# Kernel optimization log

Measured on AMD Instinct MI355X. Metric: run time of the kernel, lower is better.

Reference implementation:

```python
import jax, jax.numpy as jnp
import numpy as np

N = 4096
IN_C, HID_C, OUT_C = 128, 256, 128


def setup_inputs() -> dict:
    key = jax.random.key(0)
    ks = jax.random.split(key, 6)
    return {
        "x": jax.random.normal(ks[0], (N, IN_C), jnp.float32),
        "attn_tensor": jax.random.normal(ks[1], (1, 12, N, N), jnp.float32),
        "agg_w": jax.random.normal(ks[2], (12,), jnp.float32),
        "agg_b": jax.random.normal(ks[3], (1,), jnp.float32),
        "W1": jax.random.normal(ks[4], (IN_C, HID_C), jnp.float32) * (IN_C ** -0.5),
        "b1": jnp.zeros((HID_C,), jnp.float32),
        "W2": jax.random.normal(ks[5], (HID_C, OUT_C), jnp.float32) * (HID_C ** -0.5),
        "b2": jnp.zeros((OUT_C,), jnp.float32),
    }


def reference(x, attn_tensor, agg_w, agg_b, W1, b1, W2, b2):
    # 1x1 conv over 12 channels -> [B, N, N]
    agg = jnp.einsum("bcuv,c->buv", attn_tensor, agg_w) + agg_b[0]
    # per-batch 0.9 quantile (torch.quantile default linear interpolation)
    thresh = jnp.quantile(agg.reshape(agg.shape[0], -1), 0.9, axis=1)
    mask = agg[0] >= thresh[0]                      # [N, N] boolean adjacency
    n = mask.shape[0]
    # dense adjacency; add remaining self-loops (PyG gcn_norm fill_value=1)
    A = jnp.maximum(mask.astype(x.dtype), jnp.eye(n, dtype=x.dtype))
    deg = A.sum(axis=0)                             # in-degree at target (col) index
    s = jnp.where(deg > 0, jax.lax.rsqrt(deg), 0.0)  # D^{-1/2}, inf -> 0

    def gcn(h, W, b):
        h = h @ W                                    # linear transform (no bias)
        # out[v] = s[v] * sum_u A[u, v] * s[u] * h[u]  (source->target flow)
        return s[:, None] * (A.T @ (s[:, None] * h)) + b

    h = jax.nn.relu(gcn(x, W1, b1))
    return gcn(h, W2, b2)
```

## Files before the change

kernel.cpp:

```cpp
#include <hip/hip_runtime.h>
#include <stdint.h>

#define N_NODES 4096
#define NNN ((int64_t)N_NODES * (int64_t)N_NODES)
#define TOTAL4 (NNN / 4)
#define NC 12
#define K0_RANK 15099493u

#define SROWS 164
#define SSTRIDE 25
#define LO_RANK 601210u
#define HI_RANK 607929u

#define M_SHIST 0
#define M_CH1   4096
#define M_CH2   4352
#define M_HB    8448
#define M_DEG   8704
#define M_CNTS  12800
#define M_BLO   13824
#define M_BHI   13825
#define M_NBEL  13826
#define M_MXM   13827
#define M_SELX  13828
#define M_WORDS 14336

#define CHUNK_V 16384

typedef __attribute__((ext_vector_type(2))) _Float16 half2v;
typedef __attribute__((ext_vector_type(4))) float f4v;

static __device__ __forceinline__ uint32_t f2key(float f) {
    uint32_t x = __float_as_uint(f);
    return (x & 0x80000000u) ? ~x : (x | 0x80000000u);
}
static __device__ __forceinline__ float key2f(uint32_t k) {
    uint32_t x = (k & 0x80000000u) ? (k & 0x7FFFFFFFu) : ~k;
    return __uint_as_float(x);
}

static __device__ __forceinline__ void select_bin(const uint32_t* __restrict__ gh,
        int nb, uint32_t target, uint32_t* hl, uint32_t* sc, uint32_t* out) {
    int t = threadIdx.x;
    int per = nb >> 8;
    for (int i = t; i < nb; i += 256) hl[i] = gh[i];
    __syncthreads();
    uint32_t p = 0;
    for (int i = 0; i < per; ++i) p += hl[t * per + i];
    sc[t] = p;
    __syncthreads();
    for (int d = 1; d < 256; d <<= 1) {
        uint32_t v = (t >= d) ? sc[t - d] : 0u;
        __syncthreads();
        sc[t] += v;
        __syncthreads();
    }
    uint32_t excl = sc[t] - p;
    if (p > 0 && target >= excl && target < excl + p) {
        uint32_t cum = excl; int b = t * per;
        while (cum + hl[b] <= target) { cum += hl[b]; ++b; }
        out[0] = (uint32_t)b; out[1] = target - cum;
    }
    __syncthreads();
}

__global__ __launch_bounds__(256) void sample_kernel(const float* __restrict__ attn,
        const float* __restrict__ w, const float* __restrict__ bb,
        uint32_t* __restrict__ meta, const float* __restrict__ x,
        _Float16* __restrict__ x_h) {
    {
        const float2* x2 = (const float2*)x;
        half2v* xh2 = (half2v*)x_h;
        for (int i = blockIdx.x * 256 + threadIdx.x; i < 262144; i += 256 * 256) {
            float2 v = x2[i];
            half2v h; h[0] = (_Float16)v.x; h[1] = (_Float16)v.y;
            xh2[i] = h;
        }
    }
    __shared__ uint32_t h[4096];
    for (int i = threadIdx.x; i < 4096; i += 256) h[i] = 0;
    float wr[NC];
#pragma unroll
    for (int c = 0; c < NC; ++c) wr[c] = w[c];
    float b0 = bb[0];
    __syncthreads();
    const f4v* a4 = (const f4v*)attn;
    for (int idx = blockIdx.x * 256 + threadIdx.x; idx < SROWS * 1024; idx += 256 * 256) {
        int r = idx >> 10;
        int64_t off = (int64_t)(r * SSTRIDE) * 1024 + (idx & 1023);
        float ax = b0, ay = b0, az = b0, aw = b0;
#pragma unroll
        for (int c = 0; c < NC; ++c) {
            f4v t = __builtin_nontemporal_load(a4 + (int64_t)c * TOTAL4 + off);
            ax += wr[c] * t.x; ay += wr[c] * t.y; az += wr[c] * t.z; aw += wr[c] * t.w;
        }
        atomicAdd(&h[f2key(ax) >> 20], 1u);
        atomicAdd(&h[f2key(ay) >> 20], 1u);
        atomicAdd(&h[f2key(az) >> 20], 1u);
        atomicAdd(&h[f2key(aw) >> 20], 1u);
    }
    __syncthreads();
    for (int i = threadIdx.x; i < 4096; i += 256) {
        uint32_t c = h[i];
        if (c) atomicAdd(&meta[M_SHIST + i], c);
    }
}

__global__ __launch_bounds__(256) void aggmask_kernel(const float* __restrict__ attn,
        const float* __restrict__ w, const float* __restrict__ bb,
        uint32_t* __restrict__ meta, uint32_t* __restrict__ M,
        float* __restrict__ candV, uint32_t* __restrict__ candC) {
    __shared__ uint32_t hl[4096];
    __shared__ uint32_t sc[256];
    __shared__ uint32_t res[2];
    __shared__ uint32_t mrow[512];
    __shared__ uint32_t candH[256];
    __shared__ uint32_t cnt, nbel;
    int t = threadIdx.x;
    select_bin(meta + M_SHIST, 4096, LO_RANK, hl, sc, res);
    uint32_t blo = res[0];
    select_bin(meta + M_SHIST, 4096, HI_RANK, hl, sc, res);
    uint32_t bhi = res[0];
    for (int i = t; i < 256; i += 256) candH[i] = 0;
    if (t == 0) {
        meta[M_BLO] = blo; meta[M_BHI] = bhi;
        cnt = 0; nbel = 0;
    }
    float wr[NC];
#pragma unroll
    for (int c = 0; c < NC; ++c) wr[c] = w[c];
    float b0 = bb[0];
    __syncthreads();
    const f4v* a4 = (const f4v*)attn;
    float*    regV = candV + (size_t)blockIdx.x * CHUNK_V;
    uint32_t* regC = candC + (size_t)blockIdx.x * CHUNK_V;
    int64_t base = (int64_t)blockIdx.x * 4096;
    int u0 = blockIdx.x * 4;
    uint32_t below_t = 0;
    for (int it = 0; it < 16; ++it) {
        int li = it * 256 + t;
        float ax = b0, ay = b0, az = b0, aw = b0;
#pragma unroll
        for (int c = 0; c < NC; ++c) {
            f4v v = __builtin_nontemporal_load(a4 + (int64_t)c * TOTAL4 + base + li);
            ax += wr[c] * v.x; ay += wr[c] * v.y; az += wr[c] * v.z; aw += wr[c] * v.w;
        }
        int u = u0 + (li >> 10);
        int vcol = (li & 1023) * 4;
        float vals[4] = {ax, ay, az, aw};
        uint32_t nib = 0;
#pragma unroll
        for (int j = 0; j < 4; ++j) {
            float val = vals[j];
            uint32_t k = f2key(val);
            uint32_t top = k >> 20;
            if ((top > bhi) || (u == vcol + j)) nib |= (1u << j);
            if (top < blo) ++below_t;
            else if (top <= bhi) {
                uint32_t p = atomicAdd(&cnt, 1u);
                regV[p] = val;
                regC[p] = ((uint32_t)u << 12) | (uint32_t)(vcol + j);
                atomicAdd(&candH[min(top - blo, 255u)], 1u);
            }
        }
        uint32_t wd = nib << ((t & 7) * 4);
        wd |= (uint32_t)__shfl_xor((int)wd, 1);
        wd |= (uint32_t)__shfl_xor((int)wd, 2);
        wd |= (uint32_t)__shfl_xor((int)wd, 4);
        if ((t & 7) == 0) mrow[li >> 3] = wd;
    }
    atomicAdd(&nbel, below_t);
    __syncthreads();
    uint32_t* Mdst = M + (size_t)blockIdx.x * 512;
    Mdst[t] = mrow[t];
    Mdst[t + 256] = mrow[t + 256];
    uint32_t c = candH[t];
    if (c) atomicAdd(&meta[M_CH1 + t], c);
    if (t == 0) {
        meta[M_CNTS + blockIdx.x] = cnt;
        if (nbel) atomicAdd(&meta[M_NBEL], nbel);
    }
}

__global__ __launch_bounds__(256) void cand1_kernel(const float* __restrict__ candV,
        uint32_t* __restrict__ meta) {
    __shared__ uint32_t hl[4096];
    __shared__ uint32_t sc[256];
    __shared__ uint32_t res[2];
    int t = threadIdx.x;
    uint32_t r = K0_RANK - meta[M_NBEL];
    uint32_t blo = meta[M_BLO];
    select_bin(meta + M_CH1, 256, r, hl, sc, res);
    uint32_t b1c = blo + res[0];
    uint32_t r1 = res[1];
    if (t == 0) { meta[M_SELX + 0] = b1c; meta[M_SELX + 1] = r1; }
    for (int i = t; i < 4096; i += 256) hl[i] = 0;
    __syncthreads();
    uint32_t n = meta[M_CNTS + blockIdx.x];
    const float* region = candV + (size_t)blockIdx.x * CHUNK_V;
    for (uint32_t i = t; i < n; i += 256) {
        uint32_t key = f2key(region[i]);
        if ((key >> 20) == b1c) atomicAdd(&hl[(key >> 8) & 0xFFFu], 1u);
    }
    __syncthreads();
    for (int i = t; i < 4096; i += 256) {
        uint32_t c = hl[i];
        if (c) atomicAdd(&meta[M_CH2 + i], c);
    }
}

__global__ __launch_bounds__(256) void cand2_kernel(const float* __restrict__ candV,
        uint32_t* __restrict__ meta) {
    __shared__ uint32_t hl[4096];
    __shared__ uint32_t sc[256];
    __shared__ uint32_t res[2];
    __shared__ uint32_t hB[256];
    __shared__ uint32_t ms;
    int t = threadIdx.x;
    uint32_t r1 = meta[M_SELX + 1];
    uint32_t b1c = meta[M_SELX + 0];
    select_bin(meta + M_CH2, 4096, r1, hl, sc, res);
    uint32_t p24 = (b1c << 12) | res[0];
    hB[t] = 0;
    if (t == 0) {
        ms = 0xFFFFFFFFu;
        meta[M_SELX + 2] = res[0]; meta[M_SELX + 3] = res[1];
    }
    uint32_t n = meta[M_CNTS + blockIdx.x];
    const float* region = candV + (size_t)blockIdx.x * CHUNK_V;
    __syncthreads();
    uint32_t mn = 0xFFFFFFFFu;
    for (uint32_t i = t; i < n; i += 256) {
        uint32_t key = f2key(region[i]);
        uint32_t hi = key >> 8;
        if (hi == p24) atomicAdd(&hB[key & 0xFFu], 1u);
        else if (hi > p24) mn = min(mn, key);
    }
    atomicMin(&ms, mn);
    __syncthreads();
    uint32_t c = hB[t];
    if (c) atomicAdd(&meta[M_HB + t], c);
    if (t == 0 && ms != 0xFFFFFFFFu) atomicMax(&meta[M_MXM], ~ms);
}

__global__ __launch_bounds__(256) void candfix_kernel(const float* __restrict__ candV,
        const uint32_t* __restrict__ candC, uint32_t* __restrict__ meta,
        uint32_t* __restrict__ M) {
    __shared__ uint32_t h[256];
    __shared__ float thr;
    int t = threadIdx.x;
    h[t] = meta[M_HB + t];
    __syncthreads();
    if (t == 0) {
        uint32_t b1c = meta[M_SELX + 0], b2c = meta[M_SELX + 2], r2 = meta[M_SELX + 3];
        uint32_t cum = 0; int b = 0;
        while (b < 255 && cum + h[b] <= r2) { cum += h[b]; ++b; }
        uint32_t key0 = (b1c << 20) | (b2c << 8) | (uint32_t)b;
        uint32_t cle = cum + h[b];
        uint32_t key1;
        if (cle >= r2 + 2u) key1 = key0;
        else {
            int nb = b + 1;
            while (nb < 256 && h[nb] == 0) ++nb;
            key1 = (nb < 256) ? ((b1c << 20) | (b2c << 8) | (uint32_t)nb) : ~meta[M_MXM];
        }
        float v0 = key2f(key0);
        float v1 = key2f(key1);
        thr = v0 + 0.5f * (v1 - v0);
        meta[M_SELX + 4] = __float_as_uint(thr);
    }
    __syncthreads();
    float th = thr;
    uint32_t n = meta[M_CNTS + blockIdx.x];
    const float*    regV = candV + (size_t)blockIdx.x * CHUNK_V;
    const uint32_t* regC = candC + (size_t)blockIdx.x * CHUNK_V;
    for (uint32_t i = t; i < n; i += 256) {
        if (regV[i] >= th) {
            uint32_t c = regC[i];
            uint32_t u = c >> 12, v = c & 0xFFFu;
            atomicOr(&M[(size_t)u * 128 + (v >> 5)], 1u << (v & 31u));
        }
    }
}

__global__ __launch_bounds__(256) void transposeB_kernel(const uint32_t* __restrict__ M,
        uint32_t* __restrict__ B, uint32_t* __restrict__ deg) {
    __shared__ uint32_t tile[4][64][2];
    int wave = threadIdx.x >> 6, lane = threadIdx.x & 63;
    int tileId = blockIdx.x * 4 + wave;
    int u0 = (tileId & 63) * 64;
    int v0 = (tileId >> 6) * 64;
    uint2 two = *(const uint2*)(M + (size_t)(u0 + lane) * 128 + (v0 >> 5));
    tile[wave][lane][0] = two.x;
    tile[wave][lane][1] = two.y;
    __syncthreads();
    int sh = lane & 31, hw = lane >> 5;
    uint32_t w0 = 0, w1 = 0;
#pragma unroll
    for (int i = 0; i < 32; ++i) {
        w0 |= ((tile[wave][i][hw] >> sh) & 1u) << i;
        w1 |= ((tile[wave][32 + i][hw] >> sh) & 1u) << i;
    }
    B[(size_t)(v0 + lane) * 128 + (u0 >> 5)]     = w0;
    B[(size_t)(v0 + lane) * 128 + (u0 >> 5) + 1] = w1;
    uint32_t d = __popc(w0) + __popc(w1);
    if (d) atomicAdd(&deg[v0 + lane], d);
}

static __device__ __forceinline__ uint32_t build_idx(const uint32_t* __restrict__ B,
                                                     int v, int t, uint16_t* idx) {
    const uint32_t* row = B + (int64_t)v * 128;
    uint32_t w0 = row[t], w1 = row[t + 64];
    uint32_t pc0 = __popc(w0), pc1 = __popc(w1);
    int s0 = (int)pc0, s1 = (int)pc1;
#pragma unroll
    for (int d = 1; d < 64; d <<= 1) {
        int a = __shfl_up(s0, d);
        int b = __shfl_up(s1, d);
        if (t >= d) { s0 += a; s1 += b; }
    }
    uint32_t tot0 = (uint32_t)__shfl(s0, 63);
    uint32_t cnt  = tot0 + (uint32_t)__shfl(s1, 63);
    uint32_t p = (uint32_t)s0 - pc0;
    uint32_t m = w0;
    int ub = t * 32;
    while (m) { int bi = __ffs(m) - 1; m &= m - 1; idx[p++] = (uint16_t)(ub + bi); }
    p = tot0 + (uint32_t)s1 - pc1;
    m = w1;
    ub = (t + 64) * 32;
    while (m) { int bi = __ffs(m) - 1; m &= m - 1; idx[p++] = (uint16_t)(ub + bi); }
    __syncthreads();
    return cnt;
}

__global__ __launch_bounds__(64) void spmmX_kernel(const uint32_t* __restrict__ B,
        const _Float16* __restrict__ x_h, const uint32_t* __restrict__ deg,
        float* __restrict__ t_out) {
    __shared__ uint16_t idx[4096];
    int v = blockIdx.x;
    int t = threadIdx.x;
    uint32_t cnt = build_idx(B, v, t, idx);
    const half2v* xp = (const half2v*)x_h;
    float ax = 0.f, ay = 0.f;
    uint32_t i = 0;
    for (; i + 8 <= cnt; i += 8) {
#pragma unroll
        for (int q = 0; q < 8; ++q) {
            int u = idx[i + q];
            float su = rsqrtf((float)deg[u]);
            half2v a = xp[u * 64 + t];
            ax += su * (float)a[0]; ay += su * (float)a[1];
        }
    }
    for (; i < cnt; ++i) {
        int u = idx[i];
        float su = rsqrtf((float)deg[u]);
        half2v a = xp[u * 64 + t];
        ax += su * (float)a[0]; ay += su * (float)a[1];
    }
    float sv = rsqrtf((float)deg[v]);
    float2 r; r.x = sv * ax; r.y = sv * ay;
    ((float2*)t_out)[(int64_t)v * 64 + t] = r;
}

__global__ __launch_bounds__(256) void mlp_kernel(const float* __restrict__ t_in,
        const float* __restrict__ W1, const float* __restrict__ b1,
        const float* __restrict__ W2, const uint32_t* __restrict__ deg,
        _Float16* __restrict__ g2) {
    __shared__ float tr[8 * 128];
    __shared__ float h1s[8 * 256];
    __shared__ float sr[8];
    int u0 = blockIdx.x * 8;
    int t = threadIdx.x;
    ((float4*)tr)[t] = ((const float4*)(t_in + (int64_t)u0 * 128))[t];
    if (t < 8) sr[t] = rsqrtf((float)deg[u0 + t]);
    __syncthreads();
    {
        float acc[8] = {0, 0, 0, 0, 0, 0, 0, 0};
        for (int k = 0; k < 128; k += 4) {
            float w0 = W1[(k + 0) * 256 + t], w1 = W1[(k + 1) * 256 + t];
            float w2 = W1[(k + 2) * 256 + t], w3 = W1[(k + 3) * 256 + t];
#pragma unroll
            for (int r = 0; r < 8; ++r) {
                float4 tv = *(const float4*)&tr[r * 128 + k];
                acc[r] += tv.x * w0 + tv.y * w1 + tv.z * w2 + tv.w * w3;
            }
        }
        float bb = b1[t];
#pragma unroll
        for (int r = 0; r < 8; ++r)
            h1s[r * 256 + t] = fmaxf(acc[r] + bb, 0.f);
    }
    __syncthreads();
    {
        int col = t & 127;
        int roff = (t >> 7) * 4;
        float acc[4] = {0, 0, 0, 0};
        for (int k = 0; k < 256; k += 4) {
            float w0 = W2[(k + 0) * 128 + col], w1 = W2[(k + 1) * 128 + col];
            float w2 = W2[(k + 2) * 128 + col], w3 = W2[(k + 3) * 128 + col];
#pragma unroll
            for (int r = 0; r < 4; ++r) {
                float4 hv = *(const float4*)&h1s[(roff + r) * 256 + k];
                acc[r] += hv.x * w0 + hv.y * w1 + hv.z * w2 + hv.w * w3;
            }
        }
#pragma unroll
        for (int r = 0; r < 4; ++r)
            g2[(int64_t)(u0 + roff + r) * 128 + col] = (_Float16)(sr[roff + r] * acc[r]);
    }
}

__global__ __launch_bounds__(64) void spmm2_kernel(const uint32_t* __restrict__ B,
        const _Float16* __restrict__ g2, const uint32_t* __restrict__ deg,
        const float* __restrict__ b2, float* __restrict__ out) {
    __shared__ uint16_t idx[4096];
    int v = blockIdx.x;
    int t = threadIdx.x;
    uint32_t cnt = build_idx(B, v, t, idx);
    const half2v* gp = (const half2v*)g2;
    float ax = 0.f, ay = 0.f;
    uint32_t i = 0;
    for (; i + 8 <= cnt; i += 8) {
#pragma unroll
        for (int q = 0; q < 8; ++q) {
            half2v a = gp[idx[i + q] * 64 + t];
            ax += (float)a[0]; ay += (float)a[1];
        }
    }
    for (; i < cnt; ++i) {
        half2v a = gp[idx[i] * 64 + t];
        ax += (float)a[0]; ay += (float)a[1];
    }
    float sv = rsqrtf((float)deg[v]);
    float2 bb = ((const float2*)b2)[t];
    float2 r;
    r.x = sv * ax + bb.x;
    r.y = sv * ay + bb.y;
    ((float2*)out)[(int64_t)v * 64 + t] = r;
}

extern "C" void kernel_launch(void* const* d_in, const int* in_sizes, int n_in,
                              void* d_out, int out_size, void* d_ws, size_t ws_size,
                              hipStream_t stream) {
    const float* x    = (const float*)d_in[0];
    const float* attn = (const float*)d_in[1];
    const float* aggw = (const float*)d_in[2];
    const float* aggb = (const float*)d_in[3];
    const float* W1   = (const float*)d_in[4];
    const float* b1   = (const float*)d_in[5];
    const float* W2   = (const float*)d_in[6];
    const float* b2   = (const float*)d_in[7];
    float* out = (float*)d_out;

    char* ws = (char*)d_ws;
    size_t OFF_META  = 0;
    size_t OFF_M     = OFF_META + 65536;
    size_t OFF_B     = OFF_M + (size_t)N_NODES * 128 * 4;
    size_t OFF_CV    = OFF_B + (size_t)N_NODES * 128 * 4;
    size_t OFF_CC    = OFF_CV + (size_t)1024 * CHUNK_V * 4;
    size_t OFF_XH    = OFF_CC + (size_t)1024 * CHUNK_V * 4;
    size_t OFF_T     = OFF_XH + (size_t)N_NODES * 128 * 2;
    size_t OFF_G2    = OFF_T + (size_t)N_NODES * 128 * 4;

    uint32_t* meta  = (uint32_t*)(ws + OFF_META);
    uint32_t* Mm    = (uint32_t*)(ws + OFF_M);
    uint32_t* Bm    = (uint32_t*)(ws + OFF_B);
    float*    candV = (float*)(ws + OFF_CV);
    uint32_t* candC = (uint32_t*)(ws + OFF_CC);
    _Float16* x_h   = (_Float16*)(ws + OFF_XH);
    float*    t_ws  = (float*)(ws + OFF_T);
    _Float16* g2    = (_Float16*)(ws + OFF_G2);
    uint32_t* deg   = meta + M_DEG;

    hipMemsetAsync(meta, 0, (size_t)M_WORDS * 4, stream);

    sample_kernel<<<256, 256, 0, stream>>>(attn, aggw, aggb, meta, x, x_h);
    aggmask_kernel<<<1024, 256, 0, stream>>>(attn, aggw, aggb, meta, Mm, candV, candC);
    cand1_kernel<<<1024, 256, 0, stream>>>(candV, meta);
    cand2_kernel<<<1024, 256, 0, stream>>>(candV, meta);
    candfix_kernel<<<1024, 256, 0, stream>>>(candV, candC, meta, Mm);
    transposeB_kernel<<<1024, 256, 0, stream>>>(Mm, Bm, deg);

    spmmX_kernel<<<N_NODES, 64, 0, stream>>>(Bm, x_h, deg, t_ws);
    mlp_kernel<<<512, 256, 0, stream>>>(t_ws, W1, b1, W2, deg, g2);
    spmm2_kernel<<<N_NODES, 64, 0, stream>>>(Bm, g2, deg, b2, out);
}
```

Measured before the change: 315.8 us.

## Move per-block redundant bin selection into last-block-done epilogues

Each stage used to have all 1024 blocks re-read the global histogram and redo the prefix-scan selection at kernel start. Now the last block to finish the previous kernel, found with an atomic completion counter, does the selection once and writes the result to meta. Later kernels only load the precomputed bins and threshold. This removes redundant global reads and block-wide scans from every block, at the cost of fences, atomic counters that must be reset between calls, and a serialized tail on a single block.

Measured after the change: 626.8 us. +98.5%, slower.

```diff
diff --git a/kernel.cpp b/kernel.cpp
--- a/kernel.cpp
+++ b/kernel.cpp
@@ -23,6 +23,10 @@
 #define M_NBEL  13826
 #define M_MXM   13827
 #define M_SELX  13828
+#define M_CTR0  13840
+#define M_CTR1  13841
+#define M_CTR2  13842
+#define M_CTR3  13843
 #define M_WORDS 14336
 
 #define CHUNK_V 16384
@@ -38,12 +42,15 @@
     uint32_t x = (k & 0x80000000u) ? (k & 0x7FFFFFFFu) : ~k;
     return __uint_as_float(x);
 }
-
-static __device__ __forceinline__ void select_bin(const uint32_t* __restrict__ gh,
+static __device__ __forceinline__ uint32_t aread(uint32_t* p) {
+    return atomicAdd(p, 0u);
+}
+
+static __device__ __forceinline__ void select_bin_a(uint32_t* gh,
         int nb, uint32_t target, uint32_t* hl, uint32_t* sc, uint32_t* out) {
     int t = threadIdx.x;
     int per = nb >> 8;
-    for (int i = t; i < nb; i += 256) hl[i] = gh[i];
+    for (int i = t; i < nb; i += 256) hl[i] = aread(&gh[i]);
     __syncthreads();
     uint32_t p = 0;
     for (int i = 0; i < per; ++i) p += hl[t * per + i];
@@ -68,31 +75,35 @@
         const float* __restrict__ w, const float* __restrict__ bb,
         uint32_t* __restrict__ meta, const float* __restrict__ x,
         _Float16* __restrict__ x_h) {
+    __shared__ uint32_t h[4096];
+    __shared__ uint32_t sc[256];
+    __shared__ uint32_t res[2];
+    __shared__ uint32_t flag;
+    int t = threadIdx.x;
     {
         const float2* x2 = (const float2*)x;
         half2v* xh2 = (half2v*)x_h;
-        for (int i = blockIdx.x * 256 + threadIdx.x; i < 262144; i += 256 * 256) {
+        for (int i = blockIdx.x * 256 + t; i < 262144; i += 256 * 256) {
             float2 v = x2[i];
-            half2v h; h[0] = (_Float16)v.x; h[1] = (_Float16)v.y;
-            xh2[i] = h;
-        }
-    }
-    __shared__ uint32_t h[4096];
-    for (int i = threadIdx.x; i < 4096; i += 256) h[i] = 0;
+            half2v hh; hh[0] = (_Float16)v.x; hh[1] = (_Float16)v.y;
+            xh2[i] = hh;
+        }
+    }
+    for (int i = t; i < 4096; i += 256) h[i] = 0;
     float wr[NC];
 #pragma unroll
     for (int c = 0; c < NC; ++c) wr[c] = w[c];
     float b0 = bb[0];
     __syncthreads();
     const f4v* a4 = (const f4v*)attn;
-    for (int idx = blockIdx.x * 256 + threadIdx.x; idx < SROWS * 1024; idx += 256 * 256) {
+    for (int idx = blockIdx.x * 256 + t; idx < SROWS * 1024; idx += 256 * 256) {
         int r = idx >> 10;
         int64_t off = (int64_t)(r * SSTRIDE) * 1024 + (idx & 1023);
         float ax = b0, ay = b0, az = b0, aw = b0;
 #pragma unroll
         for (int c = 0; c < NC; ++c) {
-            f4v t = __builtin_nontemporal_load(a4 + (int64_t)c * TOTAL4 + off);
-            ax += wr[c] * t.x; ay += wr[c] * t.y; az += wr[c] * t.z; aw += wr[c] * t.w;
+            f4v tv = __builtin_nontemporal_load(a4 + (int64_t)c * TOTAL4 + off);
+            ax += wr[c] * tv.x; ay += wr[c] * tv.y; az += wr[c] * tv.z; aw += wr[c] * tv.w;
         }
         atomicAdd(&h[f2key(ax) >> 20], 1u);
         atomicAdd(&h[f2key(ay) >> 20], 1u);
@@ -100,9 +111,20 @@
         atomicAdd(&h[f2key(aw) >> 20], 1u);
     }
     __syncthreads();
-    for (int i = threadIdx.x; i < 4096; i += 256) {
+    for (int i = t; i < 4096; i += 256) {
         uint32_t c = h[i];
         if (c) atomicAdd(&meta[M_SHIST + i], c);
+    }
+    __syncthreads();
+    __threadfence();
+    if (t == 0) flag = (atomicAdd(&meta[M_CTR0], 1u) == 255u) ? 1u : 0u;
+    __syncthreads();
+    if (flag) {
+        select_bin_a(meta + M_SHIST, 4096, LO_RANK, h, sc, res);
+        if (t == 0) meta[M_BLO] = res[0];
+        __syncthreads();
+        select_bin_a(meta + M_SHIST, 4096, HI_RANK, h, sc, res);
+        if (t == 0) meta[M_BHI] = res[0];
     }
 }
 
@@ -110,26 +132,19 @@
         const float* __restrict__ w, const float* __restrict__ bb,
         uint32_t* __restrict__ meta, uint32_t* __restrict__ M,
         float* __restrict__ candV, uint32_t* __restrict__ candC) {
-    __shared__ uint32_t hl[4096];
+    __shared__ uint32_t mrow[512];
+    __shared__ uint32_t candH[256];
     __shared__ uint32_t sc[256];
     __shared__ uint32_t res[2];
-    __shared__ uint32_t mrow[512];
-    __shared__ uint32_t candH[256];
-    __shared__ uint32_t cnt, nbel;
-    int t = threadIdx.x;
-    select_bin(meta + M_SHIST, 4096, LO_RANK, hl, sc, res);
-    uint32_t blo = res[0];
-    select_bin(meta + M_SHIST, 4096, HI_RANK, hl, sc, res);
-    uint32_t bhi = res[0];
-    for (int i = t; i < 256; i += 256) candH[i] = 0;
-    if (t == 0) {
-        meta[M_BLO] = blo; meta[M_BHI] = bhi;
-        cnt = 0; nbel = 0;
-    }
+    __shared__ uint32_t cnt, nbel, flag;
+    int t = threadIdx.x;
+    candH[t] = 0;
+    if (t == 0) { cnt = 0; nbel = 0; }
     float wr[NC];
 #pragma unroll
     for (int c = 0; c < NC; ++c) wr[c] = w[c];
     float b0 = bb[0];
+    uint32_t blo = meta[M_BLO], bhi = meta[M_BHI];
     __syncthreads();
     const f4v* a4 = (const f4v*)attn;
     float*    regV = candV + (size_t)blockIdx.x * CHUNK_V;
@@ -180,6 +195,18 @@
         meta[M_CNTS + blockIdx.x] = cnt;
         if (nbel) atomicAdd(&meta[M_NBEL], nbel);
     }
+    __syncthreads();
+    __threadfence();
+    if (t == 0) flag = (atomicAdd(&meta[M_CTR1], 1u) == 1023u) ? 1u : 0u;
+    __syncthreads();
+    if (flag) {
+        uint32_t r = K0_RANK - aread(&meta[M_NBEL]);
+        select_bin_a(meta + M_CH1, 256, r, candH, sc, res);
+        if (t == 0) {
+            meta[M_SELX + 0] = meta[M_BLO] + res[0];
+            meta[M_SELX + 1] = res[1];
+        }
+    }
 }
 
 __global__ __launch_bounds__(256) void cand1_kernel(const float* __restrict__ candV,
@@ -187,13 +214,9 @@
     __shared__ uint32_t hl[4096];
     __shared__ uint32_t sc[256];
     __shared__ uint32_t res[2];
-    int t = threadIdx.x;
-    uint32_t r = K0_RANK - meta[M_NBEL];
-    uint32_t blo = meta[M_BLO];
-    select_bin(meta + M_CH1, 256, r, hl, sc, res);
-    uint32_t b1c = blo + res[0];
-    uint32_t r1 = res[1];
-    if (t == 0) { meta[M_SELX + 0] = b1c; meta[M_SELX + 1] = r1; }
+    __shared__ uint32_t flag;
+    int t = threadIdx.x;
+    uint32_t b1c = meta[M_SELX + 0];
     for (int i = t; i < 4096; i += 256) hl[i] = 0;
     __syncthreads();
     uint32_t n = meta[M_CNTS + blockIdx.x];
@@ -207,25 +230,27 @@
         uint32_t c = hl[i];
         if (c) atomicAdd(&meta[M_CH2 + i], c);
     }
+    __syncthreads();
+    __threadfence();
+    if (t == 0) flag = (atomicAdd(&meta[M_CTR2], 1u) == 1023u) ? 1u : 0u;
+    __syncthreads();
+    if (flag) {
+        uint32_t r1 = meta[M_SELX + 1];
+        select_bin_a(meta + M_CH2, 4096, r1, hl, sc, res);
+        if (t == 0) { meta[M_SELX + 2] = res[0]; meta[M_SELX + 3] = res[1]; }
+    }
 }
 
 __global__ __launch_bounds__(256) void cand2_kernel(const float* __restrict__ candV,
         uint32_t* __restrict__ meta) {
-    __shared__ uint32_t hl[4096];
-    __shared__ uint32_t sc[256];
-    __shared__ uint32_t res[2];
     __shared__ uint32_t hB[256];
-    __shared__ uint32_t ms;
-    int t = threadIdx.x;
-    uint32_t r1 = meta[M_SELX + 1];
+    __shared__ uint32_t ms, flag;
+    int t = threadIdx.x;
     uint32_t b1c = meta[M_SELX + 0];
-    select_bin(meta + M_CH2, 4096, r1, hl, sc, res);
-    uint32_t p24 = (b1c << 12) | res[0];
+    uint32_t b2c = meta[M_SELX + 2];
+    uint32_t p24 = (b1c << 12) | b2c;
     hB[t] = 0;
-    if (t == 0) {
-        ms = 0xFFFFFFFFu;
-        meta[M_SELX + 2] = res[0]; meta[M_SELX + 3] = res[1];
-    }
+    if (t == 0) ms = 0xFFFFFFFFu;
     uint32_t n = meta[M_CNTS + blockIdx.x];
     const float* region = candV + (size_t)blockIdx.x * CHUNK_V;
     __syncthreads();
@@ -241,36 +266,40 @@
     uint32_t c = hB[t];
     if (c) atomicAdd(&meta[M_HB + t], c);
     if (t == 0 && ms != 0xFFFFFFFFu) atomicMax(&meta[M_MXM], ~ms);
+    __syncthreads();
+    __threadfence();
+    if (t == 0) flag = (atomicAdd(&meta[M_CTR3], 1u) == 1023u) ? 1u : 0u;
+    __syncthreads();
+    if (flag) {
+        hB[t] = aread(&meta[M_HB + t]);
+        __syncthreads();
+        if (t == 0) {
+            uint32_t r2 = meta[M_SELX + 3];
+            uint32_t cum = 0; int b = 0;
+            while (b < 255 && cum + hB[b] <= r2) { cum += hB[b]; ++b; }
+            uint32_t key0 = (b1c << 20) | (b2c << 8) | (uint32_t)b;
+            uint32_t cle = cum + hB[b];
+            uint32_t key1;
+            if (cle >= r2 + 2u) key1 = key0;
+            else {
+                int nb = b + 1;
+                while (nb < 256 && hB[nb] == 0) ++nb;
+                key1 = (nb < 256) ? ((b1c << 20) | (b2c << 8) | (uint32_t)nb)
+                                  : ~aread(&meta[M_MXM]);
+            }
+            float v0 = key2f(key0);
+            float v1 = key2f(key1);
+            float thr = v0 + 0.5f * (v1 - v0);
+            meta[M_SELX + 4] = __float_as_uint(thr);
+        }
+    }
 }
 
 __global__ __launch_bounds__(256) void candfix_kernel(const float* __restrict__ candV,
-        const uint32_t* __restrict__ candC, uint32_t* __restrict__ meta,
+        const uint32_t* __restrict__ candC, const uint32_t* __restrict__ meta,
         uint32_t* __restrict__ M) {
-    __shared__ uint32_t h[256];
-    __shared__ float thr;
-    int t = threadIdx.x;
-    h[t] = meta[M_HB + t];
-    __syncthreads();
-    if (t == 0) {
-        uint32_t b1c = meta[M_SELX + 0], b2c = meta[M_SELX + 2], r2 = meta[M_SELX + 3];
-        uint32_t cum = 0; int b = 0;
-        while (b < 255 && cum + h[b] <= r2) { cum += h[b]; ++b; }
-        uint32_t key0 = (b1c << 20) | (b2c << 8) | (uint32_t)b;
-        uint32_t cle = cum + h[b];
-        uint32_t key1;
-        if (cle >= r2 + 2u) key1 = key0;
-        else {
-            int nb = b + 1;
-            while (nb < 256 && h[nb] == 0) ++nb;
-            key1 = (nb < 256) ? ((b1c << 20) | (b2c << 8) | (uint32_t)nb) : ~meta[M_MXM];
-        }
-        float v0 = key2f(key0);
-        float v1 = key2f(key1);
-        thr = v0 + 0.5f * (v1 - v0);
-        meta[M_SELX + 4] = __float_as_uint(thr);
-    }
-    __syncthreads();
-    float th = thr;
+    int t = threadIdx.x;
+    float th = __uint_as_float(meta[M_SELX + 4]);
     uint32_t n = meta[M_CNTS + blockIdx.x];
     const float*    regV = candV + (size_t)blockIdx.x * CHUNK_V;
     const uint32_t* regC = candC + (size_t)blockIdx.x * CHUNK_V;
```
